# Kernel optimization log

Hardware: AMD Instinct MI355X
Metric: run time of the kernel (lower is better)

Reference implementation:

```python
import jax, jax.numpy as jnp
import numpy as np
import math

D_MODEL, N_HEADS, D_HEAD, D_MLP = 768, 12, 64, 3072
EPS = 1e-5
IGNORE = -100000.0


def _ln(x, w, b):
    mu = jnp.mean(x, axis=-1, keepdims=True)
    xc = x - mu
    scale = jnp.sqrt(jnp.mean(xc * xc, axis=-1, keepdims=True) + EPS)
    return (xc / scale) * w + b


def _gelu_new(x):
    # GPT-2 'new' gelu
    return 0.5 * x * (1.0 + jnp.tanh(jnp.sqrt(2.0 / jnp.pi) * (x + 0.044715 * x ** 3)))


def setup_inputs() -> dict:
    key = jax.random.key(0)
    ks = jax.random.split(key, 12)
    std = 0.02
    inp = {
        "resid_pre": jax.random.normal(ks[0], (8, 1024, D_MODEL), jnp.float32),
        "W_Q": jax.random.normal(ks[1], (N_HEADS, D_MODEL, D_HEAD), jnp.float32) * std,
        "b_Q": jnp.zeros((N_HEADS, D_HEAD), jnp.float32),
        "W_K": jax.random.normal(ks[2], (N_HEADS, D_MODEL, D_HEAD), jnp.float32) * std,
        "b_K": jnp.zeros((N_HEADS, D_HEAD), jnp.float32),
        "W_V": jax.random.normal(ks[3], (N_HEADS, D_MODEL, D_HEAD), jnp.float32) * std,
        "b_V": jnp.zeros((N_HEADS, D_HEAD), jnp.float32),
        "W_O": jax.random.normal(ks[4], (N_HEADS, D_HEAD, D_MODEL), jnp.float32) * std,
        "b_O": jnp.zeros((D_MODEL,), jnp.float32),
        "ln1_w": jnp.ones((D_MODEL,), jnp.float32),
        "ln1_b": jnp.zeros((D_MODEL,), jnp.float32),
        "ln2_w": jnp.ones((D_MODEL,), jnp.float32),
        "ln2_b": jnp.zeros((D_MODEL,), jnp.float32),
        "W_in": jax.random.normal(ks[5], (D_MODEL, D_MLP), jnp.float32) * std,
        "b_in": jnp.zeros((D_MLP,), jnp.float32),
        "W_out": jax.random.normal(ks[6], (D_MLP, D_MODEL), jnp.float32) * std,
        "b_out": jnp.zeros((D_MODEL,), jnp.float32),
    }
    return inp


def reference(resid_pre, W_Q, b_Q, W_K, b_K, W_V, b_V, W_O, b_O,
              ln1_w, ln1_b, ln2_w, ln2_b, W_in, b_in, W_out, b_out):
    # ---- ln1 + attention ----
    n = _ln(resid_pre, ln1_w, ln1_b)  # [b, s, d]; broadcast over heads in einsums
    q = jnp.einsum('bsd,hde->bshe', n, W_Q) + b_Q
    k = jnp.einsum('bsd,hde->bshe', n, W_K) + b_K
    v = jnp.einsum('bsd,hde->bshe', n, W_V) + b_V
    scores = jnp.einsum('bqhe,bkhe->bhqk', q, k) / math.sqrt(D_HEAD)
    S = scores.shape[-1]
    causal = jnp.triu(jnp.ones((S, S), dtype=bool), k=1)
    scores = jnp.where(causal, IGNORE, scores)
    pattern = jax.nn.softmax(scores, axis=-1)
    z = jnp.einsum('bhqk,bkhe->bqhe', pattern, v)
    # per-head output with b_O / n_heads each (as in source), then summed over heads
    attn_per_head = jnp.einsum('bqhe,hed->bqhd', z, W_O) + b_O / N_HEADS
    attn_out = attn_per_head.sum(axis=2)  # [b, s, d]
    resid_mid = resid_pre + attn_out
    # ---- ln2 + mlp ----
    n2 = _ln(resid_mid, ln2_w, ln2_b)
    pre = jnp.einsum('bsd,dm->bsm', n2, W_in) + b_in
    post = _gelu_new(pre)
    mlp_out = jnp.einsum('bsm,md->bsd', post, W_out) + b_out
    return resid_mid + mlp_out
```

## Files before the change

kernel.cpp:

```cpp
#include <hip/hip_runtime.h>
#include <hip/hip_bf16.h>

typedef unsigned short u16;
typedef float f32x4 __attribute__((ext_vector_type(4)));
typedef __bf16 bf16x8 __attribute__((ext_vector_type(8)));
typedef unsigned short u16x8 __attribute__((ext_vector_type(8)));
typedef unsigned short u16x4 __attribute__((ext_vector_type(4)));

__device__ __forceinline__ float b2f(u16 u) {
    unsigned v = ((unsigned)u) << 16;
    return __builtin_bit_cast(float, v);
}
__device__ __forceinline__ u16 f2b(float f) {
    unsigned u = __builtin_bit_cast(unsigned, f);
    u += 0x7fffu + ((u >> 16) & 1u);
    return (u16)(u >> 16);
}
__device__ __forceinline__ bf16x8 ldfrag(const u16* p) {
    return __builtin_bit_cast(bf16x8, *(const u16x8*)p);
}
__device__ __forceinline__ f32x4 mfma16(bf16x8 a, bf16x8 b, f32x4 c) {
    return __builtin_amdgcn_mfma_f32_16x16x32_bf16(a, b, c, 0, 0, 0);
}
__device__ __forceinline__ void gload_lds16(const u16* g, u16* l) {
    __builtin_amdgcn_global_load_lds(
        (const __attribute__((address_space(1))) unsigned int*)(g),
        (__attribute__((address_space(3))) unsigned int*)(l), 16, 0, 0);
}

#define T_TOK 8192
#define DM 768
#define NH 12
#define DH 64
#define DMLP 3072
#define SEQ 1024
#define QKV_LD 2304
#define QK_LD 1536

#define OFF_WQKV ((size_t)0)
#define OFF_WO   (OFF_WQKV + (size_t)2304*768)
#define OFF_WIN  (OFF_WO   + (size_t)768*768)
#define OFF_WOUT (OFF_WIN  + (size_t)768*3072)
#define OFF_BQKV (OFF_WOUT + (size_t)3072*768)
#define P0       (OFF_BQKV + (size_t)4608)

#define SZ_N    ((size_t)T_TOK*DM)
#define SZ_QKV  ((size_t)T_TOK*QKV_LD)
#define A_NBUF   (P0)
#define A_QKV    (P0 + SZ_N)
#define A_Z      (P0 + SZ_N + SZ_QKV)
#define A_N2     (P0)
#define A_POST   (P0 + SZ_N)
#define PATHA_BYTES (((size_t)(P0 + SZ_N + SZ_QKV + SZ_N)) * 2)
#define B_Z      (P0)
#define B_QKVB   (P0 + SZ_N)
#define B_NBUF   (B_QKVB + (size_t)SEQ*QKV_LD)
#define B_N2     (P0)
#define B_POSTC  (P0 + SZ_N)

#define PR0 (2304*768)
#define PR1 (768*768)
#define PR2 (768*3072)
#define PR3 (3072*768)
#define PREP_TOTAL (PR0+PR1+PR2+PR3+2304)

__global__ __launch_bounds__(256) void prep_kernel(
    const float* __restrict__ WQ, const float* __restrict__ WK, const float* __restrict__ WV,
    const float* __restrict__ WO, const float* __restrict__ Win, const float* __restrict__ Wout,
    const float* __restrict__ bQ, const float* __restrict__ bK, const float* __restrict__ bV,
    u16* __restrict__ Wqkv_t, u16* __restrict__ Wo_t, u16* __restrict__ Win_t,
    u16* __restrict__ Wout_t, float* __restrict__ bias_qkv)
{
    int idx = blockIdx.x * 256 + threadIdx.x;
    if (idx < PR0) {
        int r = idx / 768, d = idx % 768;
        int which = r / 768;
        int he = r % 768;
        int h = he >> 6, e = he & 63;
        const float* W = (which == 0) ? WQ : ((which == 1) ? WK : WV);
        Wqkv_t[idx] = f2b(W[h * 49152 + d * 64 + e]);
    } else if (idx < PR0 + PR1) {
        int o = idx - PR0;
        int d = o / 768, he = o % 768;
        Wo_t[o] = f2b(WO[he * 768 + d]);
    } else if (idx < PR0 + PR1 + PR2) {
        int o = idx - PR0 - PR1;
        int m = o / 768, d = o % 768;
        Win_t[o] = f2b(Win[d * 3072 + m]);
    } else if (idx < PR0 + PR1 + PR2 + PR3) {
        int o = idx - PR0 - PR1 - PR2;
        int d = o / 3072, m = o % 3072;
        Wout_t[o] = f2b(Wout[m * 768 + d]);
    } else if (idx < PREP_TOTAL) {
        int j = idx - (PR0 + PR1 + PR2 + PR3);
        bias_qkv[j] = (j < 768) ? bQ[j] : ((j < 1536) ? bK[j - 768] : bV[j - 1536]);
    }
}

__global__ __launch_bounds__(256) void ln_kernel(
    const float* __restrict__ x, const float* __restrict__ w,
    const float* __restrict__ bb, u16* __restrict__ out)
{
    __shared__ float red[4];
    size_t base = (size_t)blockIdx.x * DM;
    int tid = threadIdx.x;
    float v0 = x[base + tid], v1 = x[base + tid + 256], v2 = x[base + tid + 512];
    float s = v0 + v1 + v2;
#pragma unroll
    for (int off = 32; off > 0; off >>= 1) s += __shfl_xor(s, off);
    if ((tid & 63) == 0) red[tid >> 6] = s;
    __syncthreads();
    float mu = (red[0] + red[1] + red[2] + red[3]) * (1.0f / 768.0f);
    v0 -= mu; v1 -= mu; v2 -= mu;
    float q = v0 * v0 + v1 * v1 + v2 * v2;
    __syncthreads();
#pragma unroll
    for (int off = 32; off > 0; off >>= 1) q += __shfl_xor(q, off);
    if ((tid & 63) == 0) red[tid >> 6] = q;
    __syncthreads();
    float var = (red[0] + red[1] + red[2] + red[3]) * (1.0f / 768.0f);
    float sc = rsqrtf(var + 1e-5f);
    out[base + tid]       = f2b(v0 * sc * w[tid]       + bb[tid]);
    out[base + tid + 256] = f2b(v1 * sc * w[tid + 256] + bb[tid + 256]);
    out[base + tid + 512] = f2b(v2 * sc * w[tid + 512] + bb[tid + 512]);
}

template <int EPI, int TM>
__global__ __launch_bounds__(256) void gemm_bt_kernel(
    const u16* __restrict__ A, const u16* __restrict__ BT,
    const float* __restrict__ bias, const float* __restrict__ aux,
    void* __restrict__ outp, int N, int K)
{
    __shared__ __align__(16) u16 As[2][TM * 32];
    __shared__ __align__(16) u16 Bs[2][128 * 32];
    const int tid = threadIdx.x;
    const int w = tid >> 6, l = tid & 63;
    const int lr = l & 15, lq = l >> 4;
    const int bm = blockIdx.x * TM, bn = blockIdx.y * 128;
    constexpr int MT = TM / 32;
    constexpr bool TR = (EPI != 4);
    const int wm = (w >> 1) * (TM / 2), wn = (w & 1) * 64;

    f32x4 acc[MT][4];
#pragma unroll
    for (int i = 0; i < MT; i++)
#pragma unroll
        for (int j = 0; j < 4; j++) acc[i][j] = f32x4{0.f, 0.f, 0.f, 0.f};

    const int srow_a = (TM == 128) ? (w * 32 + (l >> 2)) : (w * 16 + (l >> 2));
    const int srow_b = w * 32 + (l >> 2);
    const int scol = (l & 3) * 8;
    const u16* Ab = A  + (size_t)(bm + srow_a) * K + scol;
    const u16* Bb = BT + (size_t)(bn + srow_b) * K + scol;
    const int asd = (TM == 128) ? w * 1024 : w * 512;
    const int bsd = w * 1024;

    const int kiter = K >> 5;
    gload_lds16(Ab, &As[0][asd]);
    if (TM == 128) gload_lds16(Ab + 16 * K, &As[0][asd + 512]);
    gload_lds16(Bb, &Bs[0][bsd]);
    gload_lds16(Bb + 16 * K, &Bs[0][bsd + 512]);
    __syncthreads();

    int cur = 0;
    for (int kk = 0; kk < kiter; ++kk) {
        if (kk + 1 < kiter) {
            const int k0 = (kk + 1) * 32;
            gload_lds16(Ab + k0, &As[cur ^ 1][asd]);
            if (TM == 128) gload_lds16(Ab + 16 * K + k0, &As[cur ^ 1][asd + 512]);
            gload_lds16(Bb + k0,          &Bs[cur ^ 1][bsd]);
            gload_lds16(Bb + 16 * K + k0, &Bs[cur ^ 1][bsd + 512]);
        }
        bf16x8 af[MT], bf[4];
#pragma unroll
        for (int mt = 0; mt < MT; mt++) af[mt] = ldfrag(&As[cur][(wm + mt * 16 + lr) * 32 + lq * 8]);
#pragma unroll
        for (int nt = 0; nt < 4; nt++) bf[nt] = ldfrag(&Bs[cur][(wn + nt * 16 + lr) * 32 + lq * 8]);
#pragma unroll
        for (int mt = 0; mt < MT; mt++)
#pragma unroll
            for (int nt = 0; nt < 4; nt++)
                acc[mt][nt] = TR ? mfma16(bf[nt], af[mt], acc[mt][nt])
                                 : mfma16(af[mt], bf[nt], acc[mt][nt]);
        __syncthreads();
        cur ^= 1;
    }

    if (EPI == 4) {
        const bool isv = (bn >= 1536);
        u16* vtg = (u16*)aux;
#pragma unroll
        for (int mt = 0; mt < MT; mt++) {
            int row0 = bm + wm + mt * 16 + lq * 4;
            if (!isv) {
#pragma unroll
                for (int r = 0; r < 4; r++) {
                    size_t ro = (size_t)(row0 + r) * QK_LD;
#pragma unroll
                    for (int nt = 0; nt < 4; nt++) {
                        int col = bn + wn + nt * 16 + lr;
                        ((u16*)outp)[ro + col] = f2b(acc[mt][nt][r] + bias[col]);
                    }
                }
            } else {
                int bloc = row0 >> 10;
                int s = row0 & 1023;
#pragma unroll
                for (int nt = 0; nt < 4; nt++) {
                    int col = bn + wn + nt * 16 + lr;
                    int he = col - 1536;
                    float bcol = bias[col];
                    u16x4 pk;
                    pk[0] = f2b(acc[mt][nt][0] + bcol);
                    pk[1] = f2b(acc[mt][nt][1] + bcol);
                    pk[2] = f2b(acc[mt][nt][2] + bcol);
                    pk[3] = f2b(acc[mt][nt][3] + bcol);
                    *(u16x4*)&vtg[(size_t)bloc * (NH * 64 * SEQ)
                                  + (size_t)he * SEQ + s] = pk;
                }
            }
        }
        return;
    }

#pragma unroll
    for (int mt = 0; mt < MT; mt++) {
        int row = bm + wm + mt * 16 + lr;
        size_t ro = (size_t)row * N;
#pragma unroll
        for (int nt = 0; nt < 4; nt++) {
            int col0 = bn + wn + nt * 16 + lq * 4;
            f32x4 v = acc[mt][nt] + *(const f32x4*)&bias[col0];
            if (EPI == 0) {
                u16x4 pk;
#pragma unroll
                for (int r = 0; r < 4; r++) pk[r] = f2b(v[r]);
                *(u16x4*)&((u16*)outp)[ro + col0] = pk;
            } else if (EPI == 2) {
                u16x4 pk;
#pragma unroll
                for (int r = 0; r < 4; r++) {
                    float x = v[r];
                    float y = 0.7978845608028654f * (x + 0.044715f * x * x * x);
                    pk[r] = f2b(x / (1.0f + __expf(-2.0f * y)));
                }
                *(u16x4*)&((u16*)outp)[ro + col0] = pk;
            } else {
                f32x4 a4 = *(const f32x4*)&aux[ro + col0];
                v += a4;
                *(f32x4*)&((float*)outp)[ro + col0] = v;
            }
        }
    }
}

__global__ __launch_bounds__(256, 5) void attn_kernel(
    const u16* __restrict__ qk, const u16* __restrict__ vtg,
    u16* __restrict__ z, int b0, int bq0)
{
    __shared__ __align__(16) u16 Ks[64 * 72];
    __shared__ __align__(16) u16 Vt[64 * 72];
    __shared__ __align__(16) u16 Ps[4][16 * 72];

    const int qt = (int)(gridDim.x - 1) - (int)blockIdx.x;
    const int bh = blockIdx.y;
    const int b = b0 + bh / NH, h = bh % NH;
    const int tid = threadIdx.x, w = tid >> 6, l = tid & 63;
    const int lr = l & 15, lq = l >> 4;
    const int qbase = qt * 64;
    const u16* qp = qk + (size_t)(b - bq0) * SEQ * QK_LD + h * 64;
    const u16* kp = qp + 768;
    const u16* vthead = vtg + ((size_t)(b - bq0) * NH + h) * (64 * SEQ);
    u16* PsW = &Ps[w][0];

    bf16x8 aq0, aq1;
    {
        const u16* qrow = qp + (size_t)(qbase + w * 16 + lr) * QK_LD + lq * 8;
        aq0 = ldfrag(qrow);
        aq1 = ldfrag(qrow + 32);
    }

    float m_i = -1e30f;
    float l_i = 0.f;
    f32x4 O[4];
#pragma unroll
    for (int i = 0; i < 4; i++) O[i] = f32x4{0.f, 0.f, 0.f, 0.f};

    const int nkt = qt + 1;
    const int srow = tid >> 2;
    const int spart = (tid & 3) * 16;

    u16x8 kreg0, kreg1, vreg0, vreg1;
    {
        const u16* ks = kp + (size_t)srow * QK_LD + spart;
        kreg0 = *(const u16x8*)ks;
        kreg1 = *(const u16x8*)(ks + 8);
        const u16* vs = vthead + (size_t)srow * SEQ + spart;
        vreg0 = *(const u16x8*)vs;
        vreg1 = *(const u16x8*)(vs + 8);
    }

    for (int kt = 0; kt < nkt; ++kt) {
        __syncthreads();
        *(u16x8*)&Ks[srow * 72 + spart]     = kreg0;
        *(u16x8*)&Ks[srow * 72 + spart + 8] = kreg1;
        *(u16x8*)&Vt[srow * 72 + spart]     = vreg0;
        *(u16x8*)&Vt[srow * 72 + spart + 8] = vreg1;
        __syncthreads();
        if (kt + 1 < nkt) {
            const u16* ks = kp + (size_t)((kt + 1) * 64 + srow) * QK_LD + spart;
            kreg0 = *(const u16x8*)ks;
            kreg1 = *(const u16x8*)(ks + 8);
            const u16* vs = vthead + (size_t)srow * SEQ + (kt + 1) * 64 + spart;
            vreg0 = *(const u16x8*)vs;
            vreg1 = *(const u16x8*)(vs + 8);
        }

        f32x4 S[4];
#pragma unroll
        for (int nt = 0; nt < 4; nt++) S[nt] = f32x4{0.f, 0.f, 0.f, 0.f};
#pragma unroll
        for (int nt = 0; nt < 4; nt++) {
            bf16x8 bk0 = ldfrag(&Ks[(nt * 16 + lr) * 72 + lq * 8]);
            bf16x8 bk1 = ldfrag(&Ks[(nt * 16 + lr) * 72 + 32 + lq * 8]);
            S[nt] = mfma16(bk0, aq0, S[nt]);
            S[nt] = mfma16(bk1, aq1, S[nt]);
        }

        const bool diag = (kt == qt);
        float mx = -1e30f;
#pragma unroll
        for (int nt = 0; nt < 4; nt++)
#pragma unroll
            for (int r = 0; r < 4; r++) {
                float sv = S[nt][r] * 0.125f;
                if (diag) sv = (nt * 16 + lq * 4 + r <= w * 16 + lr) ? sv : -1e30f;
                S[nt][r] = sv;
                mx = fmaxf(mx, sv);
            }
        mx = fmaxf(mx, __shfl_xor(mx, 16));
        mx = fmaxf(mx, __shfl_xor(mx, 32));
        float mn = fmaxf(m_i, mx);
        float alpha = __expf(m_i - mn);
        m_i = mn;
        float rs = 0.f;
#pragma unroll
        for (int nt = 0; nt < 4; nt++) {
            u16x4 pk;
#pragma unroll
            for (int r = 0; r < 4; r++) {
                float pe = __expf(S[nt][r] - mn);
                rs += pe;
                pk[r] = f2b(pe);
            }
            *(u16x4*)&PsW[lr * 72 + nt * 16 + lq * 4] = pk;
        }
        rs += __shfl_xor(rs, 16);
        rs += __shfl_xor(rs, 32);
        l_i = l_i * alpha + rs;

#pragma unroll
        for (int r = 0; r < 4; r++) {
            float ar = __shfl(alpha, (l & 48) | (lq * 4 + r));
            O[0][r] *= ar; O[1][r] *= ar; O[2][r] *= ar; O[3][r] *= ar;
        }

#pragma unroll
        for (int kq = 0; kq < 2; kq++) {
            bf16x8 ap = ldfrag(&PsW[lr * 72 + kq * 32 + lq * 8]);
#pragma unroll
            for (int ot = 0; ot < 4; ot++) {
                bf16x8 bv = ldfrag(&Vt[(ot * 16 + lr) * 72 + kq * 32 + lq * 8]);
                O[ot] = mfma16(ap, bv, O[ot]);
            }
        }
    }

    float li[4];
#pragma unroll
    for (int r = 0; r < 4; r++)
        li[r] = __shfl(l_i, (l & 48) | (lq * 4 + r));
#pragma unroll
    for (int ot = 0; ot < 4; ot++)
#pragma unroll
        for (int r = 0; r < 4; r++) {
            int q = qbase + w * 16 + lq * 4 + r;
            size_t t = (size_t)b * SEQ + q;
            z[t * DM + h * 64 + ot * 16 + lr] = f2b(O[ot][r] / li[r]);
        }
}

extern "C" void kernel_launch(void* const* d_in, const int* in_sizes, int n_in,
                              void* d_out, int out_size, void* d_ws, size_t ws_size,
                              hipStream_t stream) {
    const float* resid_pre = (const float*)d_in[0];
    const float* W_Q  = (const float*)d_in[1];
    const float* b_Q  = (const float*)d_in[2];
    const float* W_K  = (const float*)d_in[3];
    const float* b_K  = (const float*)d_in[4];
    const float* W_V  = (const float*)d_in[5];
    const float* b_V  = (const float*)d_in[6];
    const float* W_O  = (const float*)d_in[7];
    const float* b_O  = (const float*)d_in[8];
    const float* ln1w = (const float*)d_in[9];
    const float* ln1b = (const float*)d_in[10];
    const float* ln2w = (const float*)d_in[11];
    const float* ln2b = (const float*)d_in[12];
    const float* W_in  = (const float*)d_in[13];
    const float* b_in  = (const float*)d_in[14];
    const float* W_out = (const float*)d_in[15];
    const float* b_out = (const float*)d_in[16];

    u16* ws16       = (u16*)d_ws;
    u16* Wqkv_t     = ws16 + OFF_WQKV;
    u16* Wo_t       = ws16 + OFF_WO;
    u16* Win_t      = ws16 + OFF_WIN;
    u16* Wout_t     = ws16 + OFF_WOUT;
    float* bias_qkv = (float*)(ws16 + OFF_BQKV);
    float* outp  = (float*)d_out;
    float* resid = (float*)d_out;

    prep_kernel<<<(PREP_TOTAL + 255) / 256, 256, 0, stream>>>(
        W_Q, W_K, W_V, W_O, W_in, W_out, b_Q, b_K, b_V,
        Wqkv_t, Wo_t, Win_t, Wout_t, bias_qkv);

    if (ws_size >= PATHA_BYTES) {
        u16* nbuf    = ws16 + A_NBUF;
        u16* qkbuf   = ws16 + A_QKV;
        u16* vtgA    = ws16 + A_QKV + (size_t)T_TOK * QK_LD;
        u16* zbuf    = ws16 + A_Z;
        u16* n2buf   = ws16 + A_N2;
        u16* postbuf = ws16 + A_POST;

        ln_kernel<<<T_TOK, 256, 0, stream>>>(resid_pre, ln1w, ln1b, nbuf);
        gemm_bt_kernel<4, 128><<<dim3(T_TOK / 128, QKV_LD / 128), 256, 0, stream>>>(
            nbuf, Wqkv_t, bias_qkv, (const float*)vtgA, qkbuf, QKV_LD, DM);
        attn_kernel<<<dim3(SEQ / 64, 8 * NH), 256, 0, stream>>>(qkbuf, vtgA, zbuf, 0, 0);
        gemm_bt_kernel<1, 64><<<dim3(T_TOK / 64, DM / 128), 256, 0, stream>>>(
            zbuf, Wo_t, b_O, resid_pre, resid, DM, DM);
        ln_kernel<<<T_TOK, 256, 0, stream>>>(resid, ln2w, ln2b, n2buf);
        gemm_bt_kernel<2, 128><<<dim3(T_TOK / 128, DMLP / 128), 256, 0, stream>>>(
            n2buf, Win_t, b_in, nullptr, postbuf, DMLP, DM);
        gemm_bt_kernel<3, 64><<<dim3(T_TOK / 64, DM / 128), 256, 0, stream>>>(
            postbuf, Wout_t, b_out, resid, outp, DM, DMLP);
    } else {
        u16* zbuf   = ws16 + B_Z;
        u16* qkb    = ws16 + B_QKVB;
        u16* vtgB   = qkb + (size_t)SEQ * QK_LD;
        u16* nbuf   = ws16 + B_NBUF;
        u16* n2buf  = ws16 + B_N2;
        u16* postc  = ws16 + B_POSTC;

        ln_kernel<<<T_TOK, 256, 0, stream>>>(resid_pre, ln1w, ln1b, nbuf);
        for (int b = 0; b < 8; b++) {
            gemm_bt_kernel<4, 128><<<dim3(SEQ / 128, QKV_LD / 128), 256, 0, stream>>>(
                nbuf + (size_t)b * SEQ * DM, Wqkv_t, bias_qkv, (const float*)vtgB, qkb, QKV_LD, DM);
            attn_kernel<<<dim3(SEQ / 64, NH), 256, 0, stream>>>(qkb, vtgB, zbuf, b, b);
        }
        gemm_bt_kernel<1, 64><<<dim3(T_TOK / 64, DM / 128), 256, 0, stream>>>(
            zbuf, Wo_t, b_O, resid_pre, resid, DM, DM);
        ln_kernel<<<T_TOK, 256, 0, stream>>>(resid, ln2w, ln2b, n2buf);
        for (int c = 0; c < 4; c++) {
            const size_t r0 = (size_t)c * 2048;
            gemm_bt_kernel<2, 128><<<dim3(2048 / 128, DMLP / 128), 256, 0, stream>>>(
                n2buf + r0 * DM, Win_t, b_in, nullptr, postc, DMLP, DM);
            gemm_bt_kernel<3, 64><<<dim3(2048 / 64, DM / 128), 256, 0, stream>>>(
                postc, Wout_t, b_out, resid + r0 * DM, outp + r0 * DM, DM, DMLP);
        }
    }
}
```

Before: 438.0 us.

## Use three-stage LDS pipeline with explicit vmcnt waits in GEMM

Moves the GEMM main loop from double buffering to a triple-buffered LDS ring, prefetching two K-tiles ahead. Explicit s_waitcnt vmcnt counts and a single barrier per iteration replace the trailing __syncthreads. The aim is to keep more global loads in flight and cut barrier stalls. It costs more shared memory per block, which may lower occupancy, and it depends on exact vmcnt counts matching the issued loads.

```diff
diff --git a/kernel.cpp b/kernel.cpp
--- a/kernel.cpp
+++ b/kernel.cpp
@@ -131,8 +131,8 @@
     const float* __restrict__ bias, const float* __restrict__ aux,
     void* __restrict__ outp, int N, int K)
 {
-    __shared__ __align__(16) u16 As[2][TM * 32];
-    __shared__ __align__(16) u16 Bs[2][128 * 32];
+    __shared__ __align__(16) u16 As[3][TM * 32];
+    __shared__ __align__(16) u16 Bs[3][128 * 32];
     const int tid = threadIdx.x;
     const int w = tid >> 6, l = tid & 63;
     const int lr = l & 15, lq = l >> 4;
@@ -156,35 +156,49 @@
     const int bsd = w * 1024;
 
     const int kiter = K >> 5;
-    gload_lds16(Ab, &As[0][asd]);
-    if (TM == 128) gload_lds16(Ab + 16 * K, &As[0][asd + 512]);
-    gload_lds16(Bb, &Bs[0][bsd]);
-    gload_lds16(Bb + 16 * K, &Bs[0][bsd + 512]);
-    __syncthreads();
+
+#define STAGE_T(kk, s)                                                      \
+    {   const int k0_ = (kk) * 32;                                          \
+        gload_lds16(Ab + k0_, &As[s][asd]);                                 \
+        if (TM == 128) gload_lds16(Ab + 16 * K + k0_, &As[s][asd + 512]);   \
+        gload_lds16(Bb + k0_,          &Bs[s][bsd]);                        \
+        gload_lds16(Bb + 16 * K + k0_, &Bs[s][bsd + 512]);  }
+
+    STAGE_T(0, 0);
+    STAGE_T(1, 1);
 
     int cur = 0;
-    for (int kk = 0; kk < kiter; ++kk) {
-        if (kk + 1 < kiter) {
-            const int k0 = (kk + 1) * 32;
-            gload_lds16(Ab + k0, &As[cur ^ 1][asd]);
-            if (TM == 128) gload_lds16(Ab + 16 * K + k0, &As[cur ^ 1][asd + 512]);
-            gload_lds16(Bb + k0,          &Bs[cur ^ 1][bsd]);
-            gload_lds16(Bb + 16 * K + k0, &Bs[cur ^ 1][bsd + 512]);
-        }
+    for (int t = 0; t < kiter; ++t) {
+        if (t + 1 < kiter) {
+            if constexpr (TM == 128) asm volatile("s_waitcnt vmcnt(4)" ::: "memory");
+            else                     asm volatile("s_waitcnt vmcnt(3)" ::: "memory");
+        } else {
+            asm volatile("s_waitcnt vmcnt(0)" ::: "memory");
+        }
+        __builtin_amdgcn_s_barrier();
+        __builtin_amdgcn_sched_barrier(0);
+
+        const u16* Asc = &As[cur][0];
+        const u16* Bsc = &Bs[cur][0];
         bf16x8 af[MT], bf[4];
 #pragma unroll
-        for (int mt = 0; mt < MT; mt++) af[mt] = ldfrag(&As[cur][(wm + mt * 16 + lr) * 32 + lq * 8]);
-#pragma unroll
-        for (int nt = 0; nt < 4; nt++) bf[nt] = ldfrag(&Bs[cur][(wn + nt * 16 + lr) * 32 + lq * 8]);
+        for (int mt = 0; mt < MT; mt++) af[mt] = ldfrag(&Asc[(wm + mt * 16 + lr) * 32 + lq * 8]);
+#pragma unroll
+        for (int nt = 0; nt < 4; nt++) bf[nt] = ldfrag(&Bsc[(wn + nt * 16 + lr) * 32 + lq * 8]);
 #pragma unroll
         for (int mt = 0; mt < MT; mt++)
 #pragma unroll
             for (int nt = 0; nt < 4; nt++)
                 acc[mt][nt] = TR ? mfma16(bf[nt], af[mt], acc[mt][nt])
                                  : mfma16(af[mt], bf[nt], acc[mt][nt]);
-        __syncthreads();
-        cur ^= 1;
-    }
+
+        if (t + 2 < kiter) {
+            int nb = cur + 2; if (nb >= 3) nb -= 3;
+            STAGE_T(t + 2, nb);
+        }
+        cur = (cur + 1 == 3) ? 0 : cur + 1;
+    }
+#undef STAGE_T
 
     if (EPI == 4) {
         const bool isv = (bn >= 1536);
```

New measurement: 423.7 us. 3.3% less time.
